# Kernel tuning notes

Measured on AMD Instinct MI355X. Metric: run time of the kernel, lower is better.

The kernel has to match this reference:

```python
import jax, jax.numpy as jnp
import numpy as np

PAD = 4  # init_kwargs pad


def setup_inputs() -> dict:
    key = jax.random.key(0)
    k1, k2 = jax.random.split(key)
    x = jax.random.normal(k1, (1024, 4, 84, 84), dtype=jnp.float32)
    shift = jax.random.randint(k2, (1024, 1, 1, 2), 0, 2 * PAD + 1, dtype=jnp.int32)
    return {"x": x, "shift": shift}


def _random_shift_aug(x, shift, pad):
    n, c, h, w = x.shape
    # replicate pad on H and W (matches F.pad(..., 'replicate'))
    xp = jnp.pad(x, ((0, 0), (0, 0), (pad, pad), (pad, pad)), mode='edge')
    Hp, Wp = h + 2 * pad, w + 2 * pad

    # base grid: normalized centers of the first w/h pixels of the padded image
    eps_x = 1.0 / Wp
    ax = jnp.linspace(-1.0 + eps_x, 1.0 - eps_x, Wp, dtype=x.dtype)[:w]  # (w,)
    eps_y = 1.0 / (h + 2 * 4)  # NOTE: original code hardcodes 4 here, not pad
    ay = jnp.linspace(-1.0 + eps_y, 1.0 - eps_y, h + 2 * 4, dtype=x.dtype)[:h]  # (h,)

    scale = jnp.asarray(2.0 / (h + 2 * pad), dtype=x.dtype)
    sx = shift[..., 0].astype(x.dtype) * scale  # (n,1,1)
    sy = shift[..., 1].astype(x.dtype) * scale  # (n,1,1)

    gx = ax[None, None, :] + sx  # (n,1,w) normalized x coords
    gy = ay[None, :, None] + sy  # (n,h,1) normalized y coords

    # grid_sample unnormalization, align_corners=False
    ix = ((gx + 1.0) * Wp - 1.0) * 0.5  # (n,1,w)
    iy = ((gy + 1.0) * Hp - 1.0) * 0.5  # (n,h,1)

    ix0f = jnp.floor(ix)
    iy0f = jnp.floor(iy)
    wx = (ix - ix0f)[..., None]  # (n,1,w,1)
    wy = (iy - iy0f)[..., None]  # (n,h,1,1)
    ix0 = ix0f.astype(jnp.int32)
    iy0 = iy0f.astype(jnp.int32)

    b = jnp.arange(n, dtype=jnp.int32)[:, None, None]  # (n,1,1)

    def corner(iyi, ixi):
        # zeros padding_mode: mask out-of-bounds taps
        valid = ((ixi >= 0) & (ixi < Wp) & (iyi >= 0) & (iyi < Hp)).astype(x.dtype)
        v = xp[b, :, jnp.clip(iyi, 0, Hp - 1), jnp.clip(ixi, 0, Wp - 1)]  # (n,h,w,c)
        return v * valid[..., None]

    v00 = corner(iy0, ix0)
    v01 = corner(iy0, ix0 + 1)
    v10 = corner(iy0 + 1, ix0)
    v11 = corner(iy0 + 1, ix0 + 1)

    out = (v00 * (1 - wy) * (1 - wx) + v01 * (1 - wy) * wx
           + v10 * wy * (1 - wx) + v11 * wy * wx)  # (n,h,w,c)
    return jnp.transpose(out, (0, 3, 1, 2))  # (n,c,h,w)


def reference(x, shift):
    return _random_shift_aug(x, shift, PAD)
```

## Files before the change

### kernel.cpp

```cpp
#include <hip/hip_runtime.h>


#define N_IMG 1024
#define C_DIM 4
#define HW 84
#define PADV 4
#define WQ 21
#define IMG_ELEMS (C_DIM * HW * HW)
#define IMG_VEC4 (IMG_ELEMS / 4)
#define TOTAL_VEC4 (N_IMG * IMG_VEC4)

__global__ __launch_bounds__(256)
void shift_aug_kernel(const float* __restrict__ x,
                      const int* __restrict__ shift,
                      float* __restrict__ out) {
    int idx4 = blockIdx.x * blockDim.x + threadIdx.x;
    if (idx4 >= TOTAL_VEC4) return;

    int n  = idx4 / IMG_VEC4;
    int r  = idx4 - n * IMG_VEC4;
    int wq = r % WQ;
    int t  = r / WQ;
    int h  = t % HW;

    int sx = shift[2 * n]     - PADV;
    int sy = shift[2 * n + 1] - PADV;

    int sh = min(max(h + sy, 0), HW - 1);

    const float* __restrict__ row =
        x + (size_t)n * IMG_ELEMS + (size_t)(t - h + sh) * HW;

    int wb = wq * 4 + sx;

    float4 v;
    if (wb >= 0 && wb + 3 <= HW - 1) {
        v.x = row[wb + 0];
        v.y = row[wb + 1];
        v.z = row[wb + 2];
        v.w = row[wb + 3];
    } else {
        v.x = row[min(max(wb + 0, 0), HW - 1)];
        v.y = row[min(max(wb + 1, 0), HW - 1)];
        v.z = row[min(max(wb + 2, 0), HW - 1)];
        v.w = row[min(max(wb + 3, 0), HW - 1)];
    }

    reinterpret_cast<float4*>(out)[idx4] = v;
}

extern "C" void kernel_launch(void* const* d_in, const int* in_sizes, int n_in,
                              void* d_out, int out_size, void* d_ws, size_t ws_size,
                              hipStream_t stream) {
    const float* x     = (const float*)d_in[0];
    const int*   shift = (const int*)d_in[1];
    float*       out   = (float*)d_out;

    const int threads = 256;
    const int blocks  = (TOTAL_VEC4 + threads - 1) / threads;
    shift_aug_kernel<<<blocks, threads, 0, stream>>>(x, shift, out);
}
```

Measured before the change: 201.6 us.

## Stage source rows in LDS with aligned float4 loads before shifted gather

Reorganizes the launch into a 2D grid of (channel-band, image) blocks where each block handles 12 rows of one channel plane. Each thread loads an aligned float4 of its clamped source row into shared memory, then after a barrier gathers the horizontally shifted, clamped values from LDS and writes a float4. This replaces the unaligned scalar global gathers with aligned vector loads and removes per-thread div/mod index math. In exchange it adds a block barrier and uses an odd block size of 252 threads.

```diff
diff --git a/kernel.cpp b/kernel.cpp
--- a/kernel.cpp
+++ b/kernel.cpp
@@ -1,52 +1,48 @@
 #include <hip/hip_runtime.h>
 
 
-#define N_IMG 1024
-#define C_DIM 4
 #define HW 84
+#define WQ 21
+#define RPB 12
 #define PADV 4
-#define WQ 21
-#define IMG_ELEMS (C_DIM * HW * HW)
-#define IMG_VEC4 (IMG_ELEMS / 4)
-#define TOTAL_VEC4 (N_IMG * IMG_VEC4)
+#define PLANE (HW * HW)
+#define IMG_ELEMS (4 * PLANE)
 
-__global__ __launch_bounds__(256)
+__global__ __launch_bounds__(WQ * RPB)
 void shift_aug_kernel(const float* __restrict__ x,
                       const int* __restrict__ shift,
                       float* __restrict__ out) {
-    int idx4 = blockIdx.x * blockDim.x + threadIdx.x;
-    if (idx4 >= TOTAL_VEC4) return;
+    __shared__ float lds[RPB][HW];
 
-    int n  = idx4 / IMG_VEC4;
-    int r  = idx4 - n * IMG_VEC4;
-    int wq = r % WQ;
-    int t  = r / WQ;
-    int h  = t % HW;
+    const int tx = threadIdx.x;
+    const int ty = threadIdx.y;
+    const int bx = blockIdx.x;
+    const int n  = blockIdx.y;
 
-    int sx = shift[2 * n]     - PADV;
-    int sy = shift[2 * n + 1] - PADV;
+    const int c    = bx / 7;
+    const int band = (bx - c * 7) * RPB;
 
-    int sh = min(max(h + sy, 0), HW - 1);
+    const int sx = shift[2 * n]     - PADV;
+    const int sy = shift[2 * n + 1] - PADV;
 
-    const float* __restrict__ row =
-        x + (size_t)n * IMG_ELEMS + (size_t)(t - h + sh) * HW;
+    const int h  = band + ty;
+    const int sh = min(max(h + sy, 0), HW - 1);
 
-    int wb = wq * 4 + sx;
+    const float* __restrict__ plane = x + (size_t)n * IMG_ELEMS + (size_t)c * PLANE;
 
+    float4 L = ((const float4*)(plane + sh * HW))[tx];
+    ((float4*)&lds[ty][0])[tx] = L;
+    __syncthreads();
+
+    const int wb = 4 * tx + sx;
     float4 v;
-    if (wb >= 0 && wb + 3 <= HW - 1) {
-        v.x = row[wb + 0];
-        v.y = row[wb + 1];
-        v.z = row[wb + 2];
-        v.w = row[wb + 3];
-    } else {
-        v.x = row[min(max(wb + 0, 0), HW - 1)];
-        v.y = row[min(max(wb + 1, 0), HW - 1)];
-        v.z = row[min(max(wb + 2, 0), HW - 1)];
-        v.w = row[min(max(wb + 3, 0), HW - 1)];
-    }
+    v.x = lds[ty][min(max(wb + 0, 0), HW - 1)];
+    v.y = lds[ty][min(max(wb + 1, 0), HW - 1)];
+    v.z = lds[ty][min(max(wb + 2, 0), HW - 1)];
+    v.w = lds[ty][min(max(wb + 3, 0), HW - 1)];
 
-    reinterpret_cast<float4*>(out)[idx4] = v;
+    float* __restrict__ oplane = out + (size_t)n * IMG_ELEMS + (size_t)c * PLANE;
+    ((float4*)(oplane + h * HW))[tx] = v;
 }
 
 extern "C" void kernel_launch(void* const* d_in, const int* in_sizes, int n_in,
@@ -56,7 +52,7 @@
     const int*   shift = (const int*)d_in[1];
     float*       out   = (float*)d_out;
 
-    const int threads = 256;
-    const int blocks  = (TOTAL_VEC4 + threads - 1) / threads;
-    shift_aug_kernel<<<blocks, threads, 0, stream>>>(x, shift, out);
+    dim3 block(WQ, RPB, 1);
+    dim3 grid(28, 1024, 1);
+    shift_aug_kernel<<<grid, block, 0, stream>>>(x, shift, out);
 }
```

New measurement: 195.5 us. 3.0% less time.
